# Kernel optimization log

Hardware: AMD Instinct MI355X
Metric: run time of the kernel (lower is better)

Reference implementation:

```python
import jax, jax.numpy as jnp
import numpy as np

RADIUS = 2.0
DECAY = 1.0


def setup_inputs() -> dict:
    key = jax.random.key(0)
    k1, k2 = jax.random.split(key)
    x = jax.random.normal(k1, (2048, 16), dtype=jnp.float32)
    data = jax.random.normal(k2, (65536, 16), dtype=jnp.float32)
    return {"x": x, "data": data}


def reference(x, data):
    # Brute-force L2 nearest-neighbor (faiss IndexFlatL2 / IVF nlist=1 == exact search)
    # dist2[q, n] = ||x_q - data_n||^2, via the expansion trick.
    x2 = jnp.sum(x * x, axis=1, keepdims=True)            # [Nq, 1]
    d2 = jnp.sum(data * data, axis=1)                      # [Nd]
    dist2 = x2 + d2[None, :] - 2.0 * (x @ data.T)          # [Nq, Nd] -- dominant traffic
    nn2 = jnp.maximum(jnp.min(dist2, axis=1), 0.0)         # clamp tiny negatives from cancellation
    dist = jnp.sqrt(jnp.maximum(nn2, 1e-12))               # sqrt of squared L2, squeeze(k=1)

    # bump_above(dist, RADIUS, DECAY):
    #   inside mask: exp(decay / (d^2 - r^2)) / exp(-decay / r^2)
    #   outside: 0
    r2 = RADIUS * RADIUS
    mask = jnp.abs(dist) < RADIUS
    denom = jnp.where(mask, dist * dist - r2, -1.0)        # safe denom outside mask
    bump = jnp.where(mask, jnp.exp(DECAY / denom + DECAY / r2), 0.0)
    return bump
```

## Files before the change

kernel.cpp:

```cpp
#include <hip/hip_runtime.h>
#include <float.h>
#include <math.h>

constexpr int NQ = 2048;
constexpr int ND = 65536;
constexpr int D  = 16;

constexpr int SCH   = 64;
constexpr int CP    = ND / SCH;
constexpr int TPW   = CP / 32;
constexpr int NPAIR = TPW / 2;

typedef short bf16x8 __attribute__((ext_vector_type(8)));
typedef float f32x16 __attribute__((ext_vector_type(16)));

__device__ __forceinline__ unsigned short f2bf(float f) {
    unsigned u = __float_as_uint(f);
    u += 0x7FFFu + ((u >> 16) & 1u);
    return (unsigned short)(u >> 16);
}
__device__ __forceinline__ float bf2f(unsigned short h) {
    return __uint_as_float(((unsigned)h) << 16);
}

__global__ __launch_bounds__(256) void pack_data(const float* __restrict__ data,
                                                 unsigned short* __restrict__ Ppk,
                                                 float* __restrict__ nhf) {
    const int p = blockIdx.x * 256 + threadIdx.x;
    const float4* r4 = (const float4*)(data + (size_t)p * D);
    float4 a = r4[0], b = r4[1], c = r4[2], e = r4[3];
    float v[16] = {a.x, a.y, a.z, a.w, b.x, b.y, b.z, b.w,
                   c.x, c.y, c.z, c.w, e.x, e.y, e.z, e.w};
    unsigned short row[32];
    float n = 0.f;
#pragma unroll
    for (int k = 0; k < 16; ++k) {
        n = fmaf(v[k], v[k], n);
        unsigned short h = f2bf(v[k]);
        row[k]      = h;
        row[16 + k] = f2bf(v[k] - bf2f(h));
    }
    uint4* w4 = (uint4*)(Ppk + (size_t)p * 32);
    const uint4* rr = (const uint4*)row;
    w4[0] = rr[0]; w4[1] = rr[1]; w4[2] = rr[2]; w4[3] = rr[3];
    nhf[p] = -0.5f * n;
}

__global__ __launch_bounds__(256, 4) void knn_mfma(const float* __restrict__ x,
                                                   const unsigned short* __restrict__ Ppk,
                                                   const float* __restrict__ nhf,
                                                   float* __restrict__ part) {
    const int tid  = threadIdx.x;
    const int w    = tid >> 6;
    const int l    = tid & 63;
    const int half = l >> 5;
    const int n31  = l & 31;
    const int qbase = blockIdx.x * 128 + w * 32;
    const int pbase = blockIdx.y * CP;

    const float* xr = x + (size_t)(qbase + n31) * D + half * 8;
    float4 x0 = *(const float4*)xr;
    float4 x1 = *(const float4*)(xr + 4);
    const float xv[8] = {x0.x, x0.y, x0.z, x0.w, x1.x, x1.y, x1.z, x1.w};
    bf16x8 axh, axl;
#pragma unroll
    for (int k = 0; k < 8; ++k) {
        unsigned short h = f2bf(xv[k]);
        axh[k] = (short)h;
        axl[k] = (short)f2bf(xv[k] - bf2f(h));
    }

    const unsigned short* bp = Ppk + (size_t)(pbase + n31) * 32 + half * 8;
    const float*          np = nhf + pbase + n31;

#define LDH(t) (*(const bf16x8*)(bp + (size_t)(t) * 1024))
#define LDL(t) (*(const bf16x8*)(bp + (size_t)(t) * 1024 + 16))
#define LDN(t) (np[(size_t)(t) * 32])

    f32x16 rbest;
#pragma unroll
    for (int r = 0; r < 16; ++r) rbest[r] = -FLT_MAX;

    auto compute_pair = [&](bf16x8 h0, bf16x8 l0, float n0,
                            bf16x8 h1, bf16x8 l1, float n1) {
        f32x16 c0, c1;
#pragma unroll
        for (int r = 0; r < 16; ++r) { c0[r] = n0; c1[r] = n1; }
        c0 = __builtin_amdgcn_mfma_f32_32x32x16_bf16(axh, h0, c0, 0, 0, 0);
        c1 = __builtin_amdgcn_mfma_f32_32x32x16_bf16(axh, h1, c1, 0, 0, 0);
        c0 = __builtin_amdgcn_mfma_f32_32x32x16_bf16(axl, h0, c0, 0, 0, 0);
        c1 = __builtin_amdgcn_mfma_f32_32x32x16_bf16(axl, h1, c1, 0, 0, 0);
        c0 = __builtin_amdgcn_mfma_f32_32x32x16_bf16(axh, l0, c0, 0, 0, 0);
        c1 = __builtin_amdgcn_mfma_f32_32x32x16_bf16(axh, l1, c1, 0, 0, 0);
#pragma unroll
        for (int r = 0; r < 16; ++r)
            rbest[r] = fmaxf(rbest[r], fmaxf(c0[r], c1[r]));
    };

    bf16x8 Ah0 = LDH(0), Al0 = LDL(0), Ah1 = LDH(1), Al1 = LDL(1);
    float  An0 = LDN(0), An1 = LDN(1);
    bf16x8 Bh0, Bl0, Bh1, Bl1;
    float  Bn0, Bn1;

    for (int p = 0; p < NPAIR; p += 2) {
        const int tB = (p + 1) * 2;
        Bh0 = LDH(tB);     Bl0 = LDL(tB);     Bn0 = LDN(tB);
        Bh1 = LDH(tB + 1); Bl1 = LDL(tB + 1); Bn1 = LDN(tB + 1);
        compute_pair(Ah0, Al0, An0, Ah1, Al1, An1);
        if (p + 2 < NPAIR) {
            const int tA = (p + 2) * 2;
            Ah0 = LDH(tA);     Al0 = LDL(tA);     An0 = LDN(tA);
            Ah1 = LDH(tA + 1); Al1 = LDL(tA + 1); An1 = LDN(tA + 1);
        }
        compute_pair(Bh0, Bl0, Bn0, Bh1, Bl1, Bn1);
    }
#undef LDH
#undef LDL
#undef LDN

#pragma unroll
    for (int r = 0; r < 16; ++r) {
        float v = rbest[r];
        v = fmaxf(v, __shfl_xor(v, 1, 32));
        v = fmaxf(v, __shfl_xor(v, 2, 32));
        v = fmaxf(v, __shfl_xor(v, 4, 32));
        v = fmaxf(v, __shfl_xor(v, 8, 32));
        v = fmaxf(v, __shfl_xor(v, 16, 32));
        rbest[r] = v;
    }
    if (n31 == 0) {
        float* pp = part + (size_t)blockIdx.y * NQ + qbase + 4 * half;
#pragma unroll
        for (int r = 0; r < 16; ++r) pp[(r & 3) + 8 * (r >> 2)] = rbest[r];
    }
}

__global__ __launch_bounds__(256) void knn_final(const float* __restrict__ x,
                                                 const float* __restrict__ part,
                                                 float* __restrict__ out) {
    const int q = blockIdx.x * 256 + threadIdx.x;
    const float4* xr = (const float4*)(x + (size_t)q * D);
    float4 a = xr[0], b = xr[1], c = xr[2], e = xr[3];
    float x2 = a.x * a.x;
    x2 = fmaf(a.y, a.y, x2); x2 = fmaf(a.z, a.z, x2); x2 = fmaf(a.w, a.w, x2);
    x2 = fmaf(b.x, b.x, x2); x2 = fmaf(b.y, b.y, x2); x2 = fmaf(b.z, b.z, x2); x2 = fmaf(b.w, b.w, x2);
    x2 = fmaf(c.x, c.x, x2); x2 = fmaf(c.y, c.y, x2); x2 = fmaf(c.z, c.z, x2); x2 = fmaf(c.w, c.w, x2);
    x2 = fmaf(e.x, e.x, x2); x2 = fmaf(e.y, e.y, x2); x2 = fmaf(e.z, e.z, x2); x2 = fmaf(e.w, e.w, x2);

    float mbest = -FLT_MAX;
#pragma unroll
    for (int cI = 0; cI < SCH; ++cI) mbest = fmaxf(mbest, part[(size_t)cI * NQ + q]);

    float nn2  = fmaxf(fmaf(-2.f, mbest, x2), 0.f);
    float dist = sqrtf(fmaxf(nn2, 1e-12f));
    float bump = 0.f;
    if (dist < 2.0f) {
        float denom = dist * dist - 4.0f;
        bump = expf(1.0f / denom + 0.25f);
    }
    out[q] = bump;
}

__global__ __launch_bounds__(256) void neg_half_norms(const float* __restrict__ data,
                                                      float* __restrict__ nhn) {
    const int p = blockIdx.x * 256 + threadIdx.x;
    const float4* r = (const float4*)(data + (size_t)p * D);
    float4 a = r[0], b = r[1], c = r[2], e = r[3];
    float n = a.x * a.x;
    n = fmaf(a.y, a.y, n); n = fmaf(a.z, a.z, n); n = fmaf(a.w, a.w, n);
    n = fmaf(b.x, b.x, n); n = fmaf(b.y, b.y, n); n = fmaf(b.z, b.z, n); n = fmaf(b.w, b.w, n);
    n = fmaf(c.x, c.x, n); n = fmaf(c.y, c.y, n); n = fmaf(c.z, c.z, n); n = fmaf(c.w, c.w, n);
    n = fmaf(e.x, e.x, n); n = fmaf(e.y, e.y, n); n = fmaf(e.z, e.z, n); n = fmaf(e.w, e.w, n);
    nhn[p] = -0.5f * n;
}

__global__ __launch_bounds__(256) void knn_partial_fb(const float* __restrict__ x,
                                                      const float* __restrict__ data,
                                                      const float* __restrict__ nhn,
                                                      float* __restrict__ part, int cp) {
    const int q     = blockIdx.x * 256 + threadIdx.x;
    const int pbase = blockIdx.y * cp;
    const float4* xr = (const float4*)(x + (size_t)q * D);
    const float4 xa = xr[0], xb = xr[1], xc = xr[2], xd = xr[3];
    const float* dp = data + (size_t)pbase * D;
    const float* np = nhn + pbase;
    float best = -FLT_MAX;
    for (int i = 0; i < cp; i += 4) {
#pragma unroll
        for (int j = 0; j < 4; ++j) {
            const float* r  = dp + (size_t)(i + j) * D;
            const float  hn = np[i + j];
            float ca = xa.x * r[0];
            ca = fmaf(xa.y, r[1], ca);  ca = fmaf(xa.z, r[2], ca);  ca = fmaf(xa.w, r[3], ca);
            ca = fmaf(xb.x, r[4], ca);  ca = fmaf(xb.y, r[5], ca);  ca = fmaf(xb.z, r[6], ca);
            ca = fmaf(xb.w, r[7], ca);
            float cb = fmaf(xc.x, r[8], hn);
            cb = fmaf(xc.y, r[9],  cb); cb = fmaf(xc.z, r[10], cb); cb = fmaf(xc.w, r[11], cb);
            cb = fmaf(xd.x, r[12], cb); cb = fmaf(xd.y, r[13], cb); cb = fmaf(xd.z, r[14], cb);
            cb = fmaf(xd.w, r[15], cb);
            best = fmaxf(best, ca + cb);
        }
    }
    part[(size_t)blockIdx.y * NQ + q] = best;
}

__global__ __launch_bounds__(256) void knn_final_fb(const float* __restrict__ x,
                                                    const float* __restrict__ part,
                                                    float* __restrict__ out, int S) {
    const int q = blockIdx.x * 256 + threadIdx.x;
    const float4* xr = (const float4*)(x + (size_t)q * D);
    float4 a = xr[0], b = xr[1], c = xr[2], e = xr[3];
    float x2 = a.x * a.x;
    x2 = fmaf(a.y, a.y, x2); x2 = fmaf(a.z, a.z, x2); x2 = fmaf(a.w, a.w, x2);
    x2 = fmaf(b.x, b.x, x2); x2 = fmaf(b.y, b.y, x2); x2 = fmaf(b.z, b.z, x2); x2 = fmaf(b.w, b.w, x2);
    x2 = fmaf(c.x, c.x, x2); x2 = fmaf(c.y, c.y, x2); x2 = fmaf(c.z, c.z, x2); x2 = fmaf(c.w, c.w, x2);
    x2 = fmaf(e.x, e.x, x2); x2 = fmaf(e.y, e.y, x2); x2 = fmaf(e.z, e.z, x2); x2 = fmaf(e.w, e.w, x2);
    float mb = -FLT_MAX;
    for (int cI = 0; cI < S; ++cI) mb = fmaxf(mb, part[(size_t)cI * NQ + q]);
    float nn2  = fmaxf(fmaf(-2.f, mb, x2), 0.f);
    float dist = sqrtf(fmaxf(nn2, 1e-12f));
    float bump = 0.f;
    if (dist < 2.0f) {
        float denom = dist * dist - 4.0f;
        bump = expf(1.0f / denom + 0.25f);
    }
    out[q] = bump;
}

extern "C" void kernel_launch(void* const* d_in, const int* in_sizes, int n_in,
                              void* d_out, int out_size, void* d_ws, size_t ws_size,
                              hipStream_t stream) {
    const float* x    = (const float*)d_in[0];
    const float* data = (const float*)d_in[1];
    float* out = (float*)d_out;

    const size_t off_nhf  = (size_t)ND * 32 * 2;
    const size_t off_part = off_nhf + (size_t)ND * 4;
    const size_t needed   = off_part + (size_t)SCH * NQ * 4;

    if (ws_size >= needed) {
        unsigned short* Ppk = (unsigned short*)d_ws;
        float* nhf  = (float*)((char*)d_ws + off_nhf);
        float* part = (float*)((char*)d_ws + off_part);

        pack_data<<<ND / 256, 256, 0, stream>>>(data, Ppk, nhf);
        knn_mfma<<<dim3(NQ / 128, SCH), 256, 0, stream>>>(x, Ppk, nhf, part);
        knn_final<<<NQ / 256, 256, 0, stream>>>(x, part, out);
    } else {
        int S = 32;
        while (S > 1 && (size_t)(ND + S * NQ) * sizeof(float) > ws_size) S >>= 1;
        const int cp = ND / S;
        float* nhn  = (float*)d_ws;
        float* part = (float*)d_ws + ND;
        neg_half_norms<<<ND / 256, 256, 0, stream>>>(data, nhn);
        knn_partial_fb<<<dim3(NQ / 256, S), 256, 0, stream>>>(x, data, nhn, part, cp);
        knn_final_fb<<<NQ / 256, 256, 0, stream>>>(x, part, out, S);
    }
}
```

Baseline: 85.05 us.

## Reuse each data tile across two query tiles per wave and double split count

Each wave now handles 64 queries (two 32-row A fragments) against a single B fragment, so every loaded data tile feeds two query tiles instead of one. This halves the global loads of packed data per query. To keep the grid size the same, the number of data chunks doubles to 128, which doubles the partial-max buffer the final kernel reads. The final reduction is split into four independent max chains for more ILP. The cost is more registers per thread for two accumulators and two A fragments, and a simpler one-tile-ahead prefetch.

```diff
diff --git a/kernel.cpp b/kernel.cpp
--- a/kernel.cpp
+++ b/kernel.cpp
@@ -6,10 +6,9 @@
 constexpr int ND = 65536;
 constexpr int D  = 16;
 
-constexpr int SCH   = 64;
-constexpr int CP    = ND / SCH;
-constexpr int TPW   = CP / 32;
-constexpr int NPAIR = TPW / 2;
+constexpr int SCH = 128;
+constexpr int CP  = ND / SCH;
+constexpr int TPW = CP / 32;
 
 typedef short bf16x8 __attribute__((ext_vector_type(8)));
 typedef float f32x16 __attribute__((ext_vector_type(16)));
@@ -55,83 +54,82 @@
     const int l    = tid & 63;
     const int half = l >> 5;
     const int n31  = l & 31;
-    const int qbase = blockIdx.x * 128 + w * 32;
+    const int qbase = blockIdx.x * 256 + w * 64;
     const int pbase = blockIdx.y * CP;
 
-    const float* xr = x + (size_t)(qbase + n31) * D + half * 8;
-    float4 x0 = *(const float4*)xr;
-    float4 x1 = *(const float4*)(xr + 4);
-    const float xv[8] = {x0.x, x0.y, x0.z, x0.w, x1.x, x1.y, x1.z, x1.w};
-    bf16x8 axh, axl;
-#pragma unroll
-    for (int k = 0; k < 8; ++k) {
-        unsigned short h = f2bf(xv[k]);
-        axh[k] = (short)h;
-        axl[k] = (short)f2bf(xv[k] - bf2f(h));
+    bf16x8 a0h, a0l, a1h, a1l;
+    {
+        const float* xr0 = x + (size_t)(qbase + n31) * D + half * 8;
+        const float* xr1 = x + (size_t)(qbase + 32 + n31) * D + half * 8;
+        float4 p0 = *(const float4*)xr0, p1 = *(const float4*)(xr0 + 4);
+        float4 q0 = *(const float4*)xr1, q1 = *(const float4*)(xr1 + 4);
+        const float v0[8] = {p0.x, p0.y, p0.z, p0.w, p1.x, p1.y, p1.z, p1.w};
+        const float v1[8] = {q0.x, q0.y, q0.z, q0.w, q1.x, q1.y, q1.z, q1.w};
+#pragma unroll
+        for (int k = 0; k < 8; ++k) {
+            unsigned short h0 = f2bf(v0[k]);
+            a0h[k] = (short)h0;
+            a0l[k] = (short)f2bf(v0[k] - bf2f(h0));
+            unsigned short h1 = f2bf(v1[k]);
+            a1h[k] = (short)h1;
+            a1l[k] = (short)f2bf(v1[k] - bf2f(h1));
+        }
     }
 
     const unsigned short* bp = Ppk + (size_t)(pbase + n31) * 32 + half * 8;
     const float*          np = nhf + pbase + n31;
 
-#define LDH(t) (*(const bf16x8*)(bp + (size_t)(t) * 1024))
-#define LDL(t) (*(const bf16x8*)(bp + (size_t)(t) * 1024 + 16))
-#define LDN(t) (np[(size_t)(t) * 32])
-
-    f32x16 rbest;
-#pragma unroll
-    for (int r = 0; r < 16; ++r) rbest[r] = -FLT_MAX;
-
-    auto compute_pair = [&](bf16x8 h0, bf16x8 l0, float n0,
-                            bf16x8 h1, bf16x8 l1, float n1) {
+    f32x16 rbest0, rbest1;
+#pragma unroll
+    for (int r = 0; r < 16; ++r) { rbest0[r] = -FLT_MAX; rbest1[r] = -FLT_MAX; }
+
+    bf16x8 bh = *(const bf16x8*)bp;
+    bf16x8 bl = *(const bf16x8*)(bp + 16);
+    float  nv = *np;
+
+    for (int t = 0; t < TPW; ++t) {
+        bf16x8 nbh, nbl; float nnv;
+        if (t + 1 < TPW) {
+            const unsigned short* nb = bp + (size_t)(t + 1) * 1024;
+            nbh = *(const bf16x8*)nb;
+            nbl = *(const bf16x8*)(nb + 16);
+            nnv = np[(size_t)(t + 1) * 32];
+        }
         f32x16 c0, c1;
 #pragma unroll
-        for (int r = 0; r < 16; ++r) { c0[r] = n0; c1[r] = n1; }
-        c0 = __builtin_amdgcn_mfma_f32_32x32x16_bf16(axh, h0, c0, 0, 0, 0);
-        c1 = __builtin_amdgcn_mfma_f32_32x32x16_bf16(axh, h1, c1, 0, 0, 0);
-        c0 = __builtin_amdgcn_mfma_f32_32x32x16_bf16(axl, h0, c0, 0, 0, 0);
-        c1 = __builtin_amdgcn_mfma_f32_32x32x16_bf16(axl, h1, c1, 0, 0, 0);
-        c0 = __builtin_amdgcn_mfma_f32_32x32x16_bf16(axh, l0, c0, 0, 0, 0);
-        c1 = __builtin_amdgcn_mfma_f32_32x32x16_bf16(axh, l1, c1, 0, 0, 0);
-#pragma unroll
-        for (int r = 0; r < 16; ++r)
-            rbest[r] = fmaxf(rbest[r], fmaxf(c0[r], c1[r]));
-    };
-
-    bf16x8 Ah0 = LDH(0), Al0 = LDL(0), Ah1 = LDH(1), Al1 = LDL(1);
-    float  An0 = LDN(0), An1 = LDN(1);
-    bf16x8 Bh0, Bl0, Bh1, Bl1;
-    float  Bn0, Bn1;
-
-    for (int p = 0; p < NPAIR; p += 2) {
-        const int tB = (p + 1) * 2;
-        Bh0 = LDH(tB);     Bl0 = LDL(tB);     Bn0 = LDN(tB);
-        Bh1 = LDH(tB + 1); Bl1 = LDL(tB + 1); Bn1 = LDN(tB + 1);
-        compute_pair(Ah0, Al0, An0, Ah1, Al1, An1);
-        if (p + 2 < NPAIR) {
-            const int tA = (p + 2) * 2;
-            Ah0 = LDH(tA);     Al0 = LDL(tA);     An0 = LDN(tA);
-            Ah1 = LDH(tA + 1); Al1 = LDL(tA + 1); An1 = LDN(tA + 1);
-        }
-        compute_pair(Bh0, Bl0, Bn0, Bh1, Bl1, Bn1);
-    }
-#undef LDH
-#undef LDL
-#undef LDN
+        for (int r = 0; r < 16; ++r) { c0[r] = nv; c1[r] = nv; }
+        c0 = __builtin_amdgcn_mfma_f32_32x32x16_bf16(a0h, bh, c0, 0, 0, 0);
+        c1 = __builtin_amdgcn_mfma_f32_32x32x16_bf16(a1h, bh, c1, 0, 0, 0);
+        c0 = __builtin_amdgcn_mfma_f32_32x32x16_bf16(a0l, bh, c0, 0, 0, 0);
+        c1 = __builtin_amdgcn_mfma_f32_32x32x16_bf16(a1l, bh, c1, 0, 0, 0);
+        c0 = __builtin_amdgcn_mfma_f32_32x32x16_bf16(a0h, bl, c0, 0, 0, 0);
+        c1 = __builtin_amdgcn_mfma_f32_32x32x16_bf16(a1h, bl, c1, 0, 0, 0);
+#pragma unroll
+        for (int r = 0; r < 16; ++r) {
+            rbest0[r] = fmaxf(rbest0[r], c0[r]);
+            rbest1[r] = fmaxf(rbest1[r], c1[r]);
+        }
+        bh = nbh; bl = nbl; nv = nnv;
+    }
 
 #pragma unroll
     for (int r = 0; r < 16; ++r) {
-        float v = rbest[r];
-        v = fmaxf(v, __shfl_xor(v, 1, 32));
-        v = fmaxf(v, __shfl_xor(v, 2, 32));
-        v = fmaxf(v, __shfl_xor(v, 4, 32));
-        v = fmaxf(v, __shfl_xor(v, 8, 32));
-        v = fmaxf(v, __shfl_xor(v, 16, 32));
-        rbest[r] = v;
+        float v0 = rbest0[r], v1 = rbest1[r];
+#pragma unroll
+        for (int m = 1; m < 32; m <<= 1) {
+            v0 = fmaxf(v0, __shfl_xor(v0, m, 32));
+            v1 = fmaxf(v1, __shfl_xor(v1, m, 32));
+        }
+        rbest0[r] = v0; rbest1[r] = v1;
     }
     if (n31 == 0) {
         float* pp = part + (size_t)blockIdx.y * NQ + qbase + 4 * half;
 #pragma unroll
-        for (int r = 0; r < 16; ++r) pp[(r & 3) + 8 * (r >> 2)] = rbest[r];
+        for (int r = 0; r < 16; ++r) {
+            const int row = (r & 3) + 8 * (r >> 2);
+            pp[row]      = rbest0[r];
+            pp[row + 32] = rbest1[r];
+        }
     }
 }
 
@@ -147,9 +145,15 @@
     x2 = fmaf(c.x, c.x, x2); x2 = fmaf(c.y, c.y, x2); x2 = fmaf(c.z, c.z, x2); x2 = fmaf(c.w, c.w, x2);
     x2 = fmaf(e.x, e.x, x2); x2 = fmaf(e.y, e.y, x2); x2 = fmaf(e.z, e.z, x2); x2 = fmaf(e.w, e.w, x2);
 
-    float mbest = -FLT_MAX;
-#pragma unroll
-    for (int cI = 0; cI < SCH; ++cI) mbest = fmaxf(mbest, part[(size_t)cI * NQ + q]);
+    float m0 = -FLT_MAX, m1 = -FLT_MAX, m2 = -FLT_MAX, m3 = -FLT_MAX;
+#pragma unroll
+    for (int cI = 0; cI < SCH; cI += 4) {
+        m0 = fmaxf(m0, part[(size_t)(cI + 0) * NQ + q]);
+        m1 = fmaxf(m1, part[(size_t)(cI + 1) * NQ + q]);
+        m2 = fmaxf(m2, part[(size_t)(cI + 2) * NQ + q]);
+        m3 = fmaxf(m3, part[(size_t)(cI + 3) * NQ + q]);
+    }
+    float mbest = fmaxf(fmaxf(m0, m1), fmaxf(m2, m3));
 
     float nn2  = fmaxf(fmaf(-2.f, mbest, x2), 0.f);
     float dist = sqrtf(fmaxf(nn2, 1e-12f));
@@ -244,7 +248,7 @@
         float* part = (float*)((char*)d_ws + off_part);
 
         pack_data<<<ND / 256, 256, 0, stream>>>(data, Ppk, nhf);
-        knn_mfma<<<dim3(NQ / 128, SCH), 256, 0, stream>>>(x, Ppk, nhf, part);
+        knn_mfma<<<dim3(NQ / 256, SCH), 256, 0, stream>>>(x, Ppk, nhf, part);
         knn_final<<<NQ / 256, 256, 0, stream>>>(x, part, out);
     } else {
         int S = 32;
```

Measured after the change: 106.9 us. 25.7% more time.

## Fuse final reduction into MFMA kernel via last-block atomic counter; stage norms in LDS

Applied to the files above, without the earlier changes.

Removes the separate knn_final launch. Each MFMA block bumps a per-query-column atomic counter, and the last block to finish reduces the partial maxima and computes the bump output. Counters are zeroed inside pack_data. The per-point norms are also staged into shared memory once per block, so the main loop no longer issues global loads for them. This adds a block-wide barrier before the loop and threadfence/atomic overhead at the end.

```diff
diff --git a/kernel.cpp b/kernel.cpp
--- a/kernel.cpp
+++ b/kernel.cpp
@@ -10,6 +10,7 @@
 constexpr int CP    = ND / SCH;
 constexpr int TPW   = CP / 32;
 constexpr int NPAIR = TPW / 2;
+constexpr int QCOLS = NQ / 128;
 
 typedef short bf16x8 __attribute__((ext_vector_type(8)));
 typedef float f32x16 __attribute__((ext_vector_type(16)));
@@ -25,7 +26,10 @@
 
 __global__ __launch_bounds__(256) void pack_data(const float* __restrict__ data,
                                                  unsigned short* __restrict__ Ppk,
-                                                 float* __restrict__ nhf) {
+                                                 float* __restrict__ nhf,
+                                                 int* __restrict__ cnt) {
+    if (blockIdx.x == 0 && threadIdx.x < QCOLS) cnt[threadIdx.x] = 0;
+
     const int p = blockIdx.x * 256 + threadIdx.x;
     const float4* r4 = (const float4*)(data + (size_t)p * D);
     float4 a = r4[0], b = r4[1], c = r4[2], e = r4[3];
@@ -49,7 +53,12 @@
 __global__ __launch_bounds__(256, 4) void knn_mfma(const float* __restrict__ x,
                                                    const unsigned short* __restrict__ Ppk,
                                                    const float* __restrict__ nhf,
-                                                   float* __restrict__ part) {
+                                                   float* __restrict__ part,
+                                                   int* __restrict__ cnt,
+                                                   float* __restrict__ out) {
+    __shared__ float snrm[CP];
+    __shared__ int   sdone;
+
     const int tid  = threadIdx.x;
     const int w    = tid >> 6;
     const int l    = tid & 63;
@@ -58,24 +67,29 @@
     const int qbase = blockIdx.x * 128 + w * 32;
     const int pbase = blockIdx.y * CP;
 
-    const float* xr = x + (size_t)(qbase + n31) * D + half * 8;
-    float4 x0 = *(const float4*)xr;
-    float4 x1 = *(const float4*)(xr + 4);
-    const float xv[8] = {x0.x, x0.y, x0.z, x0.w, x1.x, x1.y, x1.z, x1.w};
+#pragma unroll
+    for (int i = 0; i < CP / 256; ++i)
+        snrm[i * 256 + tid] = nhf[pbase + i * 256 + tid];
+
     bf16x8 axh, axl;
-#pragma unroll
-    for (int k = 0; k < 8; ++k) {
-        unsigned short h = f2bf(xv[k]);
-        axh[k] = (short)h;
-        axl[k] = (short)f2bf(xv[k] - bf2f(h));
+    {
+        const float* xr = x + (size_t)(qbase + n31) * D + half * 8;
+        float4 x0 = *(const float4*)xr;
+        float4 x1 = *(const float4*)(xr + 4);
+        const float xv[8] = {x0.x, x0.y, x0.z, x0.w, x1.x, x1.y, x1.z, x1.w};
+#pragma unroll
+        for (int k = 0; k < 8; ++k) {
+            unsigned short h = f2bf(xv[k]);
+            axh[k] = (short)h;
+            axl[k] = (short)f2bf(xv[k] - bf2f(h));
+        }
     }
 
     const unsigned short* bp = Ppk + (size_t)(pbase + n31) * 32 + half * 8;
-    const float*          np = nhf + pbase + n31;
 
 #define LDH(t) (*(const bf16x8*)(bp + (size_t)(t) * 1024))
 #define LDL(t) (*(const bf16x8*)(bp + (size_t)(t) * 1024 + 16))
-#define LDN(t) (np[(size_t)(t) * 32])
+#define LDN(t) (snrm[(t) * 32 + n31])
 
     f32x16 rbest;
 #pragma unroll
@@ -98,9 +112,12 @@
     };
 
     bf16x8 Ah0 = LDH(0), Al0 = LDL(0), Ah1 = LDH(1), Al1 = LDL(1);
-    float  An0 = LDN(0), An1 = LDN(1);
     bf16x8 Bh0, Bl0, Bh1, Bl1;
-    float  Bn0, Bn1;
+
+    __syncthreads();
+
+    float An0 = LDN(0), An1 = LDN(1);
+    float Bn0, Bn1;
 
     for (int p = 0; p < NPAIR; p += 2) {
         const int tB = (p + 1) * 2;
@@ -121,11 +138,8 @@
 #pragma unroll
     for (int r = 0; r < 16; ++r) {
         float v = rbest[r];
-        v = fmaxf(v, __shfl_xor(v, 1, 32));
-        v = fmaxf(v, __shfl_xor(v, 2, 32));
-        v = fmaxf(v, __shfl_xor(v, 4, 32));
-        v = fmaxf(v, __shfl_xor(v, 8, 32));
-        v = fmaxf(v, __shfl_xor(v, 16, 32));
+#pragma unroll
+        for (int m = 1; m < 32; m <<= 1) v = fmaxf(v, __shfl_xor(v, m, 32));
         rbest[r] = v;
     }
     if (n31 == 0) {
@@ -133,32 +147,46 @@
 #pragma unroll
         for (int r = 0; r < 16; ++r) pp[(r & 3) + 8 * (r >> 2)] = rbest[r];
     }
-}
-
-__global__ __launch_bounds__(256) void knn_final(const float* __restrict__ x,
-                                                 const float* __restrict__ part,
-                                                 float* __restrict__ out) {
-    const int q = blockIdx.x * 256 + threadIdx.x;
-    const float4* xr = (const float4*)(x + (size_t)q * D);
-    float4 a = xr[0], b = xr[1], c = xr[2], e = xr[3];
-    float x2 = a.x * a.x;
-    x2 = fmaf(a.y, a.y, x2); x2 = fmaf(a.z, a.z, x2); x2 = fmaf(a.w, a.w, x2);
-    x2 = fmaf(b.x, b.x, x2); x2 = fmaf(b.y, b.y, x2); x2 = fmaf(b.z, b.z, x2); x2 = fmaf(b.w, b.w, x2);
-    x2 = fmaf(c.x, c.x, x2); x2 = fmaf(c.y, c.y, x2); x2 = fmaf(c.z, c.z, x2); x2 = fmaf(c.w, c.w, x2);
-    x2 = fmaf(e.x, e.x, x2); x2 = fmaf(e.y, e.y, x2); x2 = fmaf(e.z, e.z, x2); x2 = fmaf(e.w, e.w, x2);
-
-    float mbest = -FLT_MAX;
-#pragma unroll
-    for (int cI = 0; cI < SCH; ++cI) mbest = fmaxf(mbest, part[(size_t)cI * NQ + q]);
-
-    float nn2  = fmaxf(fmaf(-2.f, mbest, x2), 0.f);
-    float dist = sqrtf(fmaxf(nn2, 1e-12f));
-    float bump = 0.f;
-    if (dist < 2.0f) {
-        float denom = dist * dist - 4.0f;
-        bump = expf(1.0f / denom + 0.25f);
-    }
-    out[q] = bump;
+
+    __threadfence();
+    __syncthreads();
+    if (tid == 0) {
+        const int old = atomicAdd(&cnt[blockIdx.x], 1);
+        sdone = (old == SCH - 1);
+    }
+    __syncthreads();
+    if (sdone) {
+        __threadfence();
+        if (tid < 128) {
+            const int q = blockIdx.x * 128 + tid;
+            float m0 = -FLT_MAX, m1 = -FLT_MAX, m2 = -FLT_MAX, m3 = -FLT_MAX;
+#pragma unroll
+            for (int cI = 0; cI < SCH; cI += 4) {
+                m0 = fmaxf(m0, part[(size_t)(cI + 0) * NQ + q]);
+                m1 = fmaxf(m1, part[(size_t)(cI + 1) * NQ + q]);
+                m2 = fmaxf(m2, part[(size_t)(cI + 2) * NQ + q]);
+                m3 = fmaxf(m3, part[(size_t)(cI + 3) * NQ + q]);
+            }
+            const float mbest = fmaxf(fmaxf(m0, m1), fmaxf(m2, m3));
+
+            const float4* xr = (const float4*)(x + (size_t)q * D);
+            float4 a = xr[0], b = xr[1], c = xr[2], e = xr[3];
+            float x2 = a.x * a.x;
+            x2 = fmaf(a.y, a.y, x2); x2 = fmaf(a.z, a.z, x2); x2 = fmaf(a.w, a.w, x2);
+            x2 = fmaf(b.x, b.x, x2); x2 = fmaf(b.y, b.y, x2); x2 = fmaf(b.z, b.z, x2); x2 = fmaf(b.w, b.w, x2);
+            x2 = fmaf(c.x, c.x, x2); x2 = fmaf(c.y, c.y, x2); x2 = fmaf(c.z, c.z, x2); x2 = fmaf(c.w, c.w, x2);
+            x2 = fmaf(e.x, e.x, x2); x2 = fmaf(e.y, e.y, x2); x2 = fmaf(e.z, e.z, x2); x2 = fmaf(e.w, e.w, x2);
+
+            float nn2  = fmaxf(fmaf(-2.f, mbest, x2), 0.f);
+            float dist = sqrtf(fmaxf(nn2, 1e-12f));
+            float bump = 0.f;
+            if (dist < 2.0f) {
+                float denom = dist * dist - 4.0f;
+                bump = expf(1.0f / denom + 0.25f);
+            }
+            out[q] = bump;
+        }
+    }
 }
 
 __global__ __launch_bounds__(256) void neg_half_norms(const float* __restrict__ data,
@@ -236,16 +264,17 @@
 
     const size_t off_nhf  = (size_t)ND * 32 * 2;
     const size_t off_part = off_nhf + (size_t)ND * 4;
-    const size_t needed   = off_part + (size_t)SCH * NQ * 4;
+    const size_t off_cnt  = off_part + (size_t)SCH * NQ * 4;
+    const size_t needed   = off_cnt + QCOLS * sizeof(int);
 
     if (ws_size >= needed) {
         unsigned short* Ppk = (unsigned short*)d_ws;
         float* nhf  = (float*)((char*)d_ws + off_nhf);
         float* part = (float*)((char*)d_ws + off_part);
-
-        pack_data<<<ND / 256, 256, 0, stream>>>(data, Ppk, nhf);
-        knn_mfma<<<dim3(NQ / 128, SCH), 256, 0, stream>>>(x, Ppk, nhf, part);
-        knn_final<<<NQ / 256, 256, 0, stream>>>(x, part, out);
+        int*   cnt  = (int*)((char*)d_ws + off_cnt);
+
+        pack_data<<<ND / 256, 256, 0, stream>>>(data, Ppk, nhf, cnt);
+        knn_mfma<<<dim3(QCOLS, SCH), 256, 0, stream>>>(x, Ppk, nhf, part, cnt, out);
     } else {
         int S = 32;
         while (S > 1 && (size_t)(ND + S * NQ) * sizeof(float) > ws_size) S >>= 1;
```

After: 160.5 us. 1.89x slower.
